# Optimization experiments

Hardware: AMD Instinct MI355X
Metric: run time of the kernel (lower is better)

## Reference

```python
import jax, jax.numpy as jnp
import numpy as np

N, M, D, DV = 8192, 8192, 512, 512

def setup_inputs() -> dict:
    key = jax.random.key(0)
    kq, kk, kv = jax.random.split(key, 3)
    return {
        "query": jax.random.normal(kq, (N, D), dtype=jnp.float32),
        "key": jax.random.normal(kk, (M, D), dtype=jnp.float32),
        "value": jax.random.normal(kv, (M, DV), dtype=jnp.float32),
    }

def reference(query, key, value):
    # scores: [N, M] = Q @ K^T (no scale, no mask, matching the torch module)
    scores = query @ key.T
    attn = jax.nn.softmax(scores, axis=-1)
    return attn @ value
```

## Files before the change

### kernel.cpp

```cpp
#include <hip/hip_runtime.h>
#include <hip/hip_fp16.h>
#include <stdint.h>

typedef _Float16 f16;
typedef _Float16 f16x8 __attribute__((ext_vector_type(8)));
typedef float    f32x4 __attribute__((ext_vector_type(4)));
typedef int      i32x4 __attribute__((ext_vector_type(4)));

#define NQ 8192
#define NK 8192
#define DD 512
#define DVV 512
#define LOG2E 1.44269504f

__device__ __forceinline__ void stage16(const void* g, void* ldsbase, int lane) {
#if __has_builtin(__builtin_amdgcn_global_load_lds)
  __builtin_amdgcn_global_load_lds((const __attribute__((address_space(1))) void*)g,
                                   (__attribute__((address_space(3))) void*)ldsbase, 16, 0, 0);
#else
  ((i32x4*)ldsbase)[lane] = *(const i32x4*)g;
#endif
}

__global__ void conv_f16k(const float* __restrict__ src, f16* __restrict__ dst, int n8) {
  int i = blockIdx.x * 256 + threadIdx.x;
  if (i >= n8) return;
  const float4* s4 = (const float4*)src;
  float4 a = s4[2 * i], b = s4[2 * i + 1];
  float vv[8] = {a.x, a.y, a.z, a.w, b.x, b.y, b.z, b.w};
  f16 h8[8];
#pragma unroll
  for (int j = 0; j < 8; ++j) h8[j] = (f16)vv[j];
  *(f16x8*)(dst + (size_t)i * 8) = *(f16x8*)h8;
}

__global__ void conv_vT(const float* __restrict__ v, f16* __restrict__ vT) {
  __shared__ float t[64][65];
  int k0 = blockIdx.x * 64, d0 = blockIdx.y * 64;
#pragma unroll
  for (int e = 0; e < 16; ++e) {
    int idx = threadIdx.x + e * 256;
    int kr = idx >> 6, dc = idx & 63;
    t[kr][dc] = v[(size_t)(k0 + kr) * DVV + d0 + dc];
  }
  __syncthreads();
  int dl = threadIdx.x >> 2, seg = (threadIdx.x & 3) * 16;
  f16 tmp[16];
#pragma unroll
  for (int c = 0; c < 16; ++c) tmp[c] = (f16)t[seg + c][dl];
  f16* dst = vT + (size_t)(d0 + dl) * NK + k0 + seg;
  *(f16x8*)dst = *(f16x8*)tmp;
  *(f16x8*)(dst + 8) = *(f16x8*)(tmp + 8);
}

__global__ __launch_bounds__(256, 3) void qk_kernel(
    const f16* __restrict__ q16, const f16* __restrict__ k16,
    f16* __restrict__ s16, float* __restrict__ pm, float* __restrict__ ps) {
  __shared__ f16 LS[16384];
  __shared__ float red[2][2][64];
  const int tid = threadIdx.x, lane = tid & 63, wid = tid >> 6;
  const int wr = wid >> 1, wc = wid & 1;
  const int bx = blockIdx.x, by = blockIdx.y;
  const int lo16 = lane & 15, hi4 = lane >> 4;

  f32x4 acc[4][4] = {};

  const int srw = lane >> 3, sc8 = (lane & 7) ^ srw;
  const f16* sptr[8];
  int dbase[8];
#pragma unroll
  for (int s = 0; s < 8; ++s) {
    int u = wid + s * 4;
    int tt = u >> 4, rb = u & 15;
    int row = rb * 8 + srw;
    sptr[s] = (tt == 0 ? q16 + (size_t)(by * 128 + row) * DD
                       : k16 + (size_t)(bx * 128 + row) * DD) + sc8 * 8;
    dbase[s] = tt * 8192 + rb * 512;
  }

  int aoff[4][2], boff[4][2];
#pragma unroll
  for (int m = 0; m < 4; ++m)
#pragma unroll
    for (int kk = 0; kk < 2; ++kk) {
      int row = wr * 64 + m * 16 + lo16;
      aoff[m][kk] = row * 64 + (((kk * 4 + hi4) ^ (row & 7)) << 3);
      int rowb = wc * 64 + m * 16 + lo16;
      boff[m][kk] = 8192 + rowb * 64 + (((kk * 4 + hi4) ^ (rowb & 7)) << 3);
    }

  for (int t = 0; t < 8; ++t) {
#pragma unroll
    for (int s = 0; s < 8; ++s) stage16(sptr[s] + t * 64, LS + dbase[s], lane);
    __syncthreads();
    f16x8 af[4][2], bf[2][4];
#pragma unroll
    for (int n = 0; n < 4; ++n)
#pragma unroll
      for (int kk = 0; kk < 2; ++kk) bf[kk][n] = *(const f16x8*)&LS[boff[n][kk]];
#pragma unroll
    for (int m = 0; m < 4; ++m)
#pragma unroll
      for (int kk = 0; kk < 2; ++kk) af[m][kk] = *(const f16x8*)&LS[aoff[m][kk]];
#pragma unroll
    for (int m = 0; m < 4; ++m)
#pragma unroll
      for (int n = 0; n < 4; ++n) {
        acc[m][n] = __builtin_amdgcn_mfma_f32_16x16x32_f16(af[m][0], bf[0][n], acc[m][n], 0, 0, 0);
        acc[m][n] = __builtin_amdgcn_mfma_f32_16x16x32_f16(af[m][1], bf[1][n], acc[m][n], 0, 0, 0);
      }
    __syncthreads();
  }

  float rmax[4][4];
#pragma unroll
  for (int i = 0; i < 4; ++i)
#pragma unroll
    for (int r = 0; r < 4; ++r) {
      float m = fmaxf(fmaxf(acc[i][0][r], acc[i][1][r]), fmaxf(acc[i][2][r], acc[i][3][r]));
#pragma unroll
      for (int d = 1; d < 16; d <<= 1) m = fmaxf(m, __shfl_xor(m, d, 64));
      rmax[i][r] = m;
    }
  if (lo16 == 0) {
#pragma unroll
    for (int i = 0; i < 4; ++i)
#pragma unroll
      for (int r = 0; r < 4; ++r) red[wr][wc][i * 16 + hi4 * 4 + r] = rmax[i][r];
  }
  __syncthreads();
  float pmv[4][4];
#pragma unroll
  for (int i = 0; i < 4; ++i)
#pragma unroll
    for (int r = 0; r < 4; ++r) {
      int rl = i * 16 + hi4 * 4 + r;
      pmv[i][r] = fmaxf(red[wr][0][rl], red[wr][1][rl]);
    }
  __syncthreads();
  float rsum[4][4];
#pragma unroll
  for (int i = 0; i < 4; ++i)
#pragma unroll
    for (int r = 0; r < 4; ++r) {
      int qloc = wr * 64 + i * 16 + hi4 * 4 + r;
      float s = 0.f;
#pragma unroll
      for (int j = 0; j < 4; ++j) {
        float p = exp2f((acc[i][j][r] - pmv[i][r]) * LOG2E);
        s += p;
        int kloc = wc * 64 + j * 16 + lo16;
        LS[qloc * 128 + (((kloc >> 3) ^ (qloc & 7)) << 3) + (kloc & 7)] = (f16)p;
      }
#pragma unroll
      for (int d = 1; d < 16; d <<= 1) s += __shfl_xor(s, d, 64);
      rsum[i][r] = s;
    }
  if (lo16 == 0) {
#pragma unroll
    for (int i = 0; i < 4; ++i)
#pragma unroll
      for (int r = 0; r < 4; ++r) red[wr][wc][i * 16 + hi4 * 4 + r] = rsum[i][r];
  }
  __syncthreads();
  if (wc == 0 && lo16 == 0) {
#pragma unroll
    for (int i = 0; i < 4; ++i)
#pragma unroll
      for (int r = 0; r < 4; ++r) {
        int rl = i * 16 + hi4 * 4 + r;
        size_t grow = (size_t)(by * 128 + wr * 64 + rl);
        pm[grow * 64 + bx] = pmv[i][r];
        ps[grow * 64 + bx] = red[wr][0][rl] + red[wr][1][rl];
      }
  }
  {
    const int q = tid >> 1, half = tid & 1;
    f16* gdst = s16 + (size_t)(by * 128 + q) * NK + bx * 128 + half * 64;
    const int sw = (q & 7) << 3;
#pragma unroll
    for (int e = 0; e < 8; ++e) {
      int k0 = half * 64 + e * 8;
      f16x8 v = *(const f16x8*)&LS[q * 128 + (((k0 >> 3) << 3) ^ sw)];
      *(f16x8*)(gdst + e * 8) = v;
    }
  }
}

__global__ void red_kernel(const float* __restrict__ pm, const float* __restrict__ ps,
                           float* __restrict__ coef) {
  int row = blockIdx.x * 4 + (threadIdx.x >> 6);
  int t = threadIdx.x & 63;
  float pmt = pm[(size_t)row * 64 + t];
  float m = pmt;
#pragma unroll
  for (int d = 1; d < 64; d <<= 1) m = fmaxf(m, __shfl_xor(m, d, 64));
  float e = exp2f((pmt - m) * LOG2E);
  float l = ps[(size_t)row * 64 + t] * e;
#pragma unroll
  for (int d = 1; d < 64; d <<= 1) l += __shfl_xor(l, d, 64);
  coef[(size_t)row * 64 + t] = e / l;
}

__global__ __launch_bounds__(256, 2) void pv_kernel(
    const f16* __restrict__ p16, const float* __restrict__ coef,
    const f16* __restrict__ vT, float* __restrict__ dst,
    int steps, size_t zstride) {
  __shared__ f16 lsA[2][128 * 64];
  __shared__ f16 lsB[2][128 * 64];
  const int tid = threadIdx.x, lane = tid & 63, wid = tid >> 6;
  const int lo16 = lane & 15, hi4 = lane >> 4;
  const int wr = wid >> 1, wc = wid & 1;
  const int bx = blockIdx.x, by = blockIdx.y, bz = blockIdx.z;
  const int g0 = bz * steps;
  f32x4 acc[4][4] = {};

  const int arow0 = tid >> 3, acol = tid & 7;
  const int srw = lane >> 3;
  const int sc = (lane & 7) ^ srw;

  f16x8 va[4];
  float scv[4];

#pragma unroll
  for (int u = 0; u < 4; ++u)
    va[u] = *(const f16x8*)(p16 + (size_t)(by * 128 + u * 32 + arow0) * NK + (size_t)g0 * 64 + acol * 8);
#pragma unroll
  for (int i = 0; i < 4; ++i) {
    int unit = wid * 4 + i;
    int row = unit * 8 + srw;
    stage16(vT + (size_t)(bx * 128 + row) * NK + (size_t)g0 * 64 + sc * 8,
            &lsB[0][unit * 512], lane);
  }
#pragma unroll
  for (int u = 0; u < 4; ++u)
    scv[u] = coef[(size_t)(by * 128 + u * 32 + arow0) * 64 + (g0 >> 1)];
#pragma unroll
  for (int u = 0; u < 4; ++u) {
    int row = u * 32 + arow0;
    f16x8 vv = va[u] * (f16)scv[u];
    *(f16x8*)&lsA[0][row * 64 + ((acol ^ (row & 7)) << 3)] = vv;
  }
  __syncthreads();

  for (int s = 0; s < steps; ++s) {
    const int cur = s & 1, nxt = cur ^ 1;
    const int g = g0 + s;
    if (s + 1 < steps) {
#pragma unroll
      for (int u = 0; u < 4; ++u)
        va[u] = *(const f16x8*)(p16 + (size_t)(by * 128 + u * 32 + arow0) * NK +
                                (size_t)(g + 1) * 64 + acol * 8);
#pragma unroll
      for (int i = 0; i < 4; ++i) {
        int unit = wid * 4 + i;
        int row = unit * 8 + srw;
        stage16(vT + (size_t)(bx * 128 + row) * NK + (size_t)(g + 1) * 64 + sc * 8,
                &lsB[nxt][unit * 512], lane);
      }
#pragma unroll
      for (int u = 0; u < 4; ++u)
        scv[u] = coef[(size_t)(by * 128 + u * 32 + arow0) * 64 + ((g + 1) >> 1)];
    }
#pragma unroll
    for (int ks = 0; ks < 2; ++ks) {
      f16x8 af[4], bf[4];
#pragma unroll
      for (int i = 0; i < 4; ++i) {
        int row = wr * 64 + i * 16 + lo16;
        af[i] = *(const f16x8*)&lsA[cur][row * 64 + (((ks * 4 + hi4) ^ (row & 7)) << 3)];
      }
#pragma unroll
      for (int j = 0; j < 4; ++j) {
        int dv = wc * 64 + j * 16 + lo16;
        bf[j] = *(const f16x8*)&lsB[cur][dv * 64 + (((ks * 4 + hi4) ^ (dv & 7)) << 3)];
      }
#pragma unroll
      for (int i = 0; i < 4; ++i)
#pragma unroll
        for (int j = 0; j < 4; ++j)
          acc[i][j] = __builtin_amdgcn_mfma_f32_16x16x32_f16(af[i], bf[j], acc[i][j], 0, 0, 0);
    }
    if (s + 1 < steps) {
#pragma unroll
      for (int u = 0; u < 4; ++u) {
        int row = u * 32 + arow0;
        f16x8 vv = va[u] * (f16)scv[u];
        *(f16x8*)&lsA[nxt][row * 64 + ((acol ^ (row & 7)) << 3)] = vv;
      }
    }
    __syncthreads();
  }

  float* o = dst + (size_t)bz * zstride;
#pragma unroll
  for (int i = 0; i < 4; ++i)
#pragma unroll
    for (int j = 0; j < 4; ++j)
#pragma unroll
      for (int r = 0; r < 4; ++r)
        o[(size_t)(by * 128 + wr * 64 + i * 16 + hi4 * 4 + r) * DVV +
          bx * 128 + wc * 64 + j * 16 + lo16] = acc[i][j][r];
}

__global__ void reduce_out(const float* __restrict__ part, float* __restrict__ out,
                           int ks, size_t n4) {
  size_t i = (size_t)blockIdx.x * 256 + threadIdx.x;
  if (i >= n4) return;
  float4 a = ((const float4*)part)[i];
  for (int z = 1; z < ks; ++z) {
    float4 b = ((const float4*)(part + z * n4 * 4))[i];
    a.x += b.x; a.y += b.y; a.z += b.z; a.w += b.w;
  }
  ((float4*)out)[i] = a;
}

__global__ void zero_out(float* o, int n) {
  int i = blockIdx.x * 256 + threadIdx.x;
  if (i < n) o[i] = 0.f;
}

extern "C" void kernel_launch(void* const* d_in, const int* in_sizes, int n_in,
                              void* d_out, int out_size, void* d_ws, size_t ws_size,
                              hipStream_t stream) {
  (void)in_sizes; (void)n_in; (void)out_size;
  const float* Q = (const float*)d_in[0];
  const float* K = (const float*)d_in[1];
  const float* V = (const float*)d_in[2];
  float* out = (float*)d_out;

  const size_t sz16 = (size_t)NK * DD * 2;
  const size_t fixedB = 2 * sz16;
  const size_t perRow = 1024 + 64 * 4 * 3 + (size_t)NK * 2;
  const size_t partB = (size_t)16384 * DVV * 4;
  int nc = 0;
  for (int cand = 8192; cand >= 1024; cand >>= 1)
    if (fixedB + (size_t)cand * perRow + partB <= ws_size) { nc = cand; break; }
  if (nc == 0) {
    zero_out<<<(NQ * DVV + 255) / 256, 256, 0, stream>>>(out, NQ * DVV);
    return;
  }
  const int ks = 16384 / nc;
  const int steps = 128 / ks;

  char* w = (char*)d_ws;
  f16* k16 = (f16*)w;
  f16* vT = (f16*)(w + sz16);
  char* p = w + fixedB;
  f16* q16 = (f16*)p;      p += (size_t)nc * 1024;
  float* pm = (float*)p;   p += (size_t)nc * 256;
  float* ps = (float*)p;   p += (size_t)nc * 256;
  float* coef = (float*)p; p += (size_t)nc * 256;
  f16* s16 = (f16*)p;      p += (size_t)nc * NK * 2;
  float* part = (float*)p;

  conv_f16k<<<NK * DD / 8 / 256, 256, 0, stream>>>(K, k16, NK * DD / 8);
  conv_vT<<<dim3(NK / 64, DVV / 64), 256, 0, stream>>>(V, vT);

  for (int c = 0; c < NQ / nc; ++c) {
    conv_f16k<<<nc * DD / 8 / 256, 256, 0, stream>>>(Q + (size_t)c * nc * DD, q16, nc * DD / 8);
    qk_kernel<<<dim3(NK / 128, nc / 128), 256, 0, stream>>>(q16, k16, s16, pm, ps);
    red_kernel<<<nc / 4, 256, 0, stream>>>(pm, ps, coef);
    pv_kernel<<<dim3(DVV / 128, nc / 128, ks), 256, 0, stream>>>(
        s16, coef, vT, part, steps, (size_t)nc * DVV);
    reduce_out<<<(int)(((size_t)nc * DVV / 4 + 255) / 256), 256, 0, stream>>>(
        part, out + (size_t)c * nc * DVV, ks, (size_t)nc * DVV / 4);
  }
}
```

Measured before the change: 274.5 us.

## Drop split-K partials in PV, use 64-row tiles and transposed softmax stats

The PV kernel no longer splits the key dimension across grid z into partial outputs that a separate reduce kernel sums. Each block now covers 64 query rows over all 128 key tiles and writes the output directly, with the grid doubled along rows to keep enough blocks. The per-tile max/sum/coef arrays are stored transposed, so PV reads coefficients with coalesced loads. This removes the partial-buffer write/read traffic and one launch, at the cost of a smaller per-block tile with less reuse of V per load and longer serial loops per block.

```diff
diff --git a/kernel.cpp b/kernel.cpp
--- a/kernel.cpp
+++ b/kernel.cpp
@@ -55,7 +55,8 @@
 
 __global__ __launch_bounds__(256, 3) void qk_kernel(
     const f16* __restrict__ q16, const f16* __restrict__ k16,
-    f16* __restrict__ s16, float* __restrict__ pm, float* __restrict__ ps) {
+    f16* __restrict__ s16, float* __restrict__ pmT, float* __restrict__ psT,
+    int nrows) {
   __shared__ f16 LS[16384];
   __shared__ float red[2][2][64];
   const int tid = threadIdx.x, lane = tid & 63, wid = tid >> 6;
@@ -170,8 +171,8 @@
       for (int r = 0; r < 4; ++r) {
         int rl = i * 16 + hi4 * 4 + r;
         size_t grow = (size_t)(by * 128 + wr * 64 + rl);
-        pm[grow * 64 + bx] = pmv[i][r];
-        ps[grow * 64 + bx] = red[wr][0][rl] + red[wr][1][rl];
+        pmT[(size_t)bx * nrows + grow] = pmv[i][r];
+        psT[(size_t)bx * nrows + grow] = red[wr][0][rl] + red[wr][1][rl];
       }
   }
   {
@@ -181,93 +182,88 @@
 #pragma unroll
     for (int e = 0; e < 8; ++e) {
       int k0 = half * 64 + e * 8;
-      f16x8 v = *(const f16x8*)&LS[q * 128 + (((k0 >> 3) << 3) ^ sw)];
+      f16x8 v = *(const f16x8*)&LS[q * 128 + (k0 ^ sw)];
       *(f16x8*)(gdst + e * 8) = v;
     }
   }
 }
 
-__global__ void red_kernel(const float* __restrict__ pm, const float* __restrict__ ps,
-                           float* __restrict__ coef) {
+__global__ void red_kernel(const float* __restrict__ pmT, const float* __restrict__ psT,
+                           float* __restrict__ coefT, int nrows) {
   int row = blockIdx.x * 4 + (threadIdx.x >> 6);
   int t = threadIdx.x & 63;
-  float pmt = pm[(size_t)row * 64 + t];
+  float pmt = pmT[(size_t)t * nrows + row];
   float m = pmt;
 #pragma unroll
   for (int d = 1; d < 64; d <<= 1) m = fmaxf(m, __shfl_xor(m, d, 64));
   float e = exp2f((pmt - m) * LOG2E);
-  float l = ps[(size_t)row * 64 + t] * e;
+  float l = psT[(size_t)t * nrows + row] * e;
 #pragma unroll
   for (int d = 1; d < 64; d <<= 1) l += __shfl_xor(l, d, 64);
-  coef[(size_t)row * 64 + t] = e / l;
+  coefT[(size_t)t * nrows + row] = e / l;
 }
 
 __global__ __launch_bounds__(256, 2) void pv_kernel(
-    const f16* __restrict__ p16, const float* __restrict__ coef,
-    const f16* __restrict__ vT, float* __restrict__ dst,
-    int steps, size_t zstride) {
-  __shared__ f16 lsA[2][128 * 64];
+    const f16* __restrict__ p16, const float* __restrict__ coefT,
+    const f16* __restrict__ vT, float* __restrict__ out, int nrows) {
+  __shared__ f16 lsA[2][64 * 64];
   __shared__ f16 lsB[2][128 * 64];
   const int tid = threadIdx.x, lane = tid & 63, wid = tid >> 6;
   const int lo16 = lane & 15, hi4 = lane >> 4;
   const int wr = wid >> 1, wc = wid & 1;
-  const int bx = blockIdx.x, by = blockIdx.y, bz = blockIdx.z;
-  const int g0 = bz * steps;
-  f32x4 acc[4][4] = {};
-
-  const int arow0 = tid >> 3, acol = tid & 7;
-  const int srw = lane >> 3;
-  const int sc = (lane & 7) ^ srw;
-
-  f16x8 va[4];
-  float scv[4];
-
-#pragma unroll
-  for (int u = 0; u < 4; ++u)
-    va[u] = *(const f16x8*)(p16 + (size_t)(by * 128 + u * 32 + arow0) * NK + (size_t)g0 * 64 + acol * 8);
-#pragma unroll
-  for (int i = 0; i < 4; ++i) {
-    int unit = wid * 4 + i;
-    int row = unit * 8 + srw;
-    stage16(vT + (size_t)(bx * 128 + row) * NK + (size_t)g0 * 64 + sc * 8,
-            &lsB[0][unit * 512], lane);
-  }
-#pragma unroll
-  for (int u = 0; u < 4; ++u)
-    scv[u] = coef[(size_t)(by * 128 + u * 32 + arow0) * 64 + (g0 >> 1)];
-#pragma unroll
-  for (int u = 0; u < 4; ++u) {
-    int row = u * 32 + arow0;
-    f16x8 vv = va[u] * (f16)scv[u];
-    *(f16x8*)&lsA[0][row * 64 + ((acol ^ (row & 7)) << 3)] = vv;
-  }
-  __syncthreads();
-
-  for (int s = 0; s < steps; ++s) {
-    const int cur = s & 1, nxt = cur ^ 1;
-    const int g = g0 + s;
-    if (s + 1 < steps) {
-#pragma unroll
-      for (int u = 0; u < 4; ++u)
-        va[u] = *(const f16x8*)(p16 + (size_t)(by * 128 + u * 32 + arow0) * NK +
-                                (size_t)(g + 1) * 64 + acol * 8);
-#pragma unroll
-      for (int i = 0; i < 4; ++i) {
-        int unit = wid * 4 + i;
-        int row = unit * 8 + srw;
-        stage16(vT + (size_t)(bx * 128 + row) * NK + (size_t)(g + 1) * 64 + sc * 8,
-                &lsB[nxt][unit * 512], lane);
-      }
-#pragma unroll
-      for (int u = 0; u < 4; ++u)
-        scv[u] = coef[(size_t)(by * 128 + u * 32 + arow0) * 64 + ((g + 1) >> 1)];
+  const int bx = blockIdx.x, by = blockIdx.y;
+  f32x4 acc[2][4] = {};
+
+  const int arow = tid >> 2, aseg = tid & 3;
+  const int srw = lane >> 3, sc8 = (lane & 7) ^ srw;
+
+  f16x8 va[2];
+  float scv;
+
+  const f16* ga0 = p16 + (size_t)(by * 64 + arow) * NK + aseg * 16;
+
+#define PV_LOADA(kt)                                                          \
+  do {                                                                        \
+    va[0] = *(const f16x8*)(ga0 + (size_t)(kt) * 64);                         \
+    va[1] = *(const f16x8*)(ga0 + (size_t)(kt) * 64 + 8);                     \
+    scv = coefT[(size_t)((kt) >> 1) * nrows + by * 64 + arow];                \
+  } while (0)
+#define PV_STGB(kt, buf)                                                      \
+  do {                                                                        \
+    _Pragma("unroll") for (int i = 0; i < 4; ++i) {                           \
+      int unit = wid * 4 + i;                                                 \
+      int row = unit * 8 + srw;                                               \
+      stage16(vT + (size_t)(bx * 128 + row) * NK + (size_t)(kt) * 64 + sc8 * 8, \
+              &lsB[buf][unit * 512], lane);                                   \
+    }                                                                         \
+  } while (0)
+#define PV_WRA(buf)                                                           \
+  do {                                                                        \
+    f16 sch = (f16)scv;                                                       \
+    _Pragma("unroll") for (int u2 = 0; u2 < 2; ++u2) {                        \
+      f16x8 vv = va[u2] * sch;                                                \
+      int u = aseg * 2 + u2;                                                  \
+      *(f16x8*)&lsA[buf][arow * 64 + ((u ^ (arow & 7)) << 3)] = vv;           \
+    }                                                                         \
+  } while (0)
+
+  PV_LOADA(0);
+  PV_STGB(0, 0);
+  PV_WRA(0);
+  __syncthreads();
+
+  for (int kt = 0; kt < 128; ++kt) {
+    const int cur = kt & 1, nxt = cur ^ 1;
+    if (kt < 127) {
+      PV_LOADA(kt + 1);
+      PV_STGB(kt + 1, nxt);
     }
 #pragma unroll
     for (int ks = 0; ks < 2; ++ks) {
-      f16x8 af[4], bf[4];
-#pragma unroll
-      for (int i = 0; i < 4; ++i) {
-        int row = wr * 64 + i * 16 + lo16;
+      f16x8 af[2], bf[4];
+#pragma unroll
+      for (int i = 0; i < 2; ++i) {
+        int row = wr * 32 + i * 16 + lo16;
         af[i] = *(const f16x8*)&lsA[cur][row * 64 + (((ks * 4 + hi4) ^ (row & 7)) << 3)];
       }
 #pragma unroll
@@ -276,43 +272,26 @@
         bf[j] = *(const f16x8*)&lsB[cur][dv * 64 + (((ks * 4 + hi4) ^ (dv & 7)) << 3)];
       }
 #pragma unroll
-      for (int i = 0; i < 4; ++i)
+      for (int i = 0; i < 2; ++i)
 #pragma unroll
         for (int j = 0; j < 4; ++j)
           acc[i][j] = __builtin_amdgcn_mfma_f32_16x16x32_f16(af[i], bf[j], acc[i][j], 0, 0, 0);
     }
-    if (s + 1 < steps) {
-#pragma unroll
-      for (int u = 0; u < 4; ++u) {
-        int row = u * 32 + arow0;
-        f16x8 vv = va[u] * (f16)scv[u];
-        *(f16x8*)&lsA[nxt][row * 64 + ((acol ^ (row & 7)) << 3)] = vv;
-      }
-    }
+    if (kt < 127) PV_WRA(nxt);
     __syncthreads();
   }
-
-  float* o = dst + (size_t)bz * zstride;
-#pragma unroll
-  for (int i = 0; i < 4; ++i)
+#undef PV_LOADA
+#undef PV_STGB
+#undef PV_WRA
+
+#pragma unroll
+  for (int i = 0; i < 2; ++i)
 #pragma unroll
     for (int j = 0; j < 4; ++j)
 #pragma unroll
       for (int r = 0; r < 4; ++r)
-        o[(size_t)(by * 128 + wr * 64 + i * 16 + hi4 * 4 + r) * DVV +
-          bx * 128 + wc * 64 + j * 16 + lo16] = acc[i][j][r];
-}
-
-__global__ void reduce_out(const float* __restrict__ part, float* __restrict__ out,
-                           int ks, size_t n4) {
-  size_t i = (size_t)blockIdx.x * 256 + threadIdx.x;
-  if (i >= n4) return;
-  float4 a = ((const float4*)part)[i];
-  for (int z = 1; z < ks; ++z) {
-    float4 b = ((const float4*)(part + z * n4 * 4))[i];
-    a.x += b.x; a.y += b.y; a.z += b.z; a.w += b.w;
-  }
-  ((float4*)out)[i] = a;
+        out[(size_t)(by * 64 + wr * 32 + i * 16 + hi4 * 4 + r) * DVV +
+            bx * 128 + wc * 64 + j * 16 + lo16] = acc[i][j][r];
 }
 
 __global__ void zero_out(float* o, int n) {
@@ -332,38 +311,32 @@
   const size_t sz16 = (size_t)NK * DD * 2;
   const size_t fixedB = 2 * sz16;
   const size_t perRow = 1024 + 64 * 4 * 3 + (size_t)NK * 2;
-  const size_t partB = (size_t)16384 * DVV * 4;
   int nc = 0;
   for (int cand = 8192; cand >= 1024; cand >>= 1)
-    if (fixedB + (size_t)cand * perRow + partB <= ws_size) { nc = cand; break; }
+    if (fixedB + (size_t)cand * perRow <= ws_size) { nc = cand; break; }
   if (nc == 0) {
     zero_out<<<(NQ * DVV + 255) / 256, 256, 0, stream>>>(out, NQ * DVV);
     return;
   }
-  const int ks = 16384 / nc;
-  const int steps = 128 / ks;
 
   char* w = (char*)d_ws;
   f16* k16 = (f16*)w;
   f16* vT = (f16*)(w + sz16);
   char* p = w + fixedB;
   f16* q16 = (f16*)p;      p += (size_t)nc * 1024;
-  float* pm = (float*)p;   p += (size_t)nc * 256;
-  float* ps = (float*)p;   p += (size_t)nc * 256;
-  float* coef = (float*)p; p += (size_t)nc * 256;
-  f16* s16 = (f16*)p;      p += (size_t)nc * NK * 2;
-  float* part = (float*)p;
+  float* pmT = (float*)p;  p += (size_t)nc * 256;
+  float* psT = (float*)p;  p += (size_t)nc * 256;
+  float* coefT = (float*)p; p += (size_t)nc * 256;
+  f16* s16 = (f16*)p;
 
   conv_f16k<<<NK * DD / 8 / 256, 256, 0, stream>>>(K, k16, NK * DD / 8);
   conv_vT<<<dim3(NK / 64, DVV / 64), 256, 0, stream>>>(V, vT);
 
   for (int c = 0; c < NQ / nc; ++c) {
     conv_f16k<<<nc * DD / 8 / 256, 256, 0, stream>>>(Q + (size_t)c * nc * DD, q16, nc * DD / 8);
-    qk_kernel<<<dim3(NK / 128, nc / 128), 256, 0, stream>>>(q16, k16, s16, pm, ps);
-    red_kernel<<<nc / 4, 256, 0, stream>>>(pm, ps, coef);
-    pv_kernel<<<dim3(DVV / 128, nc / 128, ks), 256, 0, stream>>>(
-        s16, coef, vT, part, steps, (size_t)nc * DVV);
-    reduce_out<<<(int)(((size_t)nc * DVV / 4 + 255) / 256), 256, 0, stream>>>(
-        part, out + (size_t)c * nc * DVV, ks, (size_t)nc * DVV / 4);
-  }
-}
+    qk_kernel<<<dim3(NK / 128, nc / 128), 256, 0, stream>>>(q16, k16, s16, pmT, psT, nc);
+    red_kernel<<<nc / 4, 256, 0, stream>>>(pmT, psT, coefT, nc);
+    pv_kernel<<<dim3(DVV / 128, nc / 64), 256, 0, stream>>>(
+        s16, coefT, vT, out + (size_t)c * nc * DVV, nc);
+  }
+}
```

New measurement: 306.8 us. 1.12x slower.
